# Kernel tuning notes

Measured on AMD Instinct MI355X. Metric: run time of the kernel, lower is better.

Reference implementation:

```python
import jax, jax.numpy as jnp
import numpy as np

MEMORY_SIZE = 512
EMBED_DIM = 768
BATCH, SEQ = 4, 8192


def setup_inputs() -> dict:
    key = jax.random.key(0)
    k1, k2 = jax.random.split(key)
    hidden_states = jax.random.normal(k1, (BATCH, SEQ, EMBED_DIM), dtype=jnp.float32)
    memory = jax.random.normal(k2, (MEMORY_SIZE, EMBED_DIM), dtype=jnp.float32)
    return {"hidden_states": hidden_states, "memory": memory}


def reference(hidden_states, memory):
    # importance[s] = mean over batch of L2 norm of hidden_states[b, s, :]
    importance = jnp.linalg.norm(hidden_states, axis=-1).mean(axis=0)  # [S]
    k = min(MEMORY_SIZE, importance.shape[0])  # static
    _, topk_idx = jax.lax.top_k(importance, k)  # [k]
    # gather per-token batch-mean vectors and scatter into first k memory slots
    mean_h = hidden_states.mean(axis=0)  # [S, D]
    new_memory = memory.at[:k].set(mean_h[topk_idx])  # [M, D]
    return new_memory
```

## Files before the change

kernel.cpp:

```cpp
#include <hip/hip_runtime.h>
#include <stdint.h>

#define S_TOK 8192
#define D_DIM 768
#define B_SZ  4
#define K_TOP 512
#define NSLICE 32
#define SLICE (S_TOK / NSLICE)

__global__ __launch_bounds__(256) void importance_kernel(const float4* __restrict__ h4,
                                                         uint32_t* __restrict__ imp_u) {
    const int D4 = D_DIM / 4;
    const size_t SB = (size_t)S_TOK * D4;
    const int wave = (blockIdx.x * blockDim.x + threadIdx.x) >> 6;
    const int lane = threadIdx.x & 63;
    const float4* r = h4 + (size_t)wave * D4 + lane;

    float4 v0 = r[0 * SB + 0],  v1 = r[0 * SB + 64],  v2 = r[0 * SB + 128];
    float4 v3 = r[1 * SB + 0],  v4 = r[1 * SB + 64],  v5 = r[1 * SB + 128];
    float4 v6 = r[2 * SB + 0],  v7 = r[2 * SB + 64],  v8 = r[2 * SB + 128];
    float4 v9 = r[3 * SB + 0],  vA = r[3 * SB + 64],  vB = r[3 * SB + 128];

    float d0 = v0.x * v0.x + v0.y * v0.y + v0.z * v0.z + v0.w * v0.w;
    float d1 = v1.x * v1.x + v1.y * v1.y + v1.z * v1.z + v1.w * v1.w;
    float d2 = v2.x * v2.x + v2.y * v2.y + v2.z * v2.z + v2.w * v2.w;
    float d3 = v3.x * v3.x + v3.y * v3.y + v3.z * v3.z + v3.w * v3.w;
    float d4 = v4.x * v4.x + v4.y * v4.y + v4.z * v4.z + v4.w * v4.w;
    float d5 = v5.x * v5.x + v5.y * v5.y + v5.z * v5.z + v5.w * v5.w;
    float d6 = v6.x * v6.x + v6.y * v6.y + v6.z * v6.z + v6.w * v6.w;
    float d7 = v7.x * v7.x + v7.y * v7.y + v7.z * v7.z + v7.w * v7.w;
    float d8 = v8.x * v8.x + v8.y * v8.y + v8.z * v8.z + v8.w * v8.w;
    float d9 = v9.x * v9.x + v9.y * v9.y + v9.z * v9.z + v9.w * v9.w;
    float dA = vA.x * vA.x + vA.y * vA.y + vA.z * vA.z + vA.w * vA.w;
    float dB = vB.x * vB.x + vB.y * vB.y + vB.z * vB.z + vB.w * vB.w;

    float a0 = d0 + d1 + d2;
    float a1 = d3 + d4 + d5;
    float a2 = d6 + d7 + d8;
    float a3 = d9 + dA + dB;

#pragma unroll
    for (int off = 32; off >= 1; off >>= 1) {
        a0 += __shfl_xor(a0, off);
        a1 += __shfl_xor(a1, off);
        a2 += __shfl_xor(a2, off);
        a3 += __shfl_xor(a3, off);
    }
    if (lane == 0) {
        float acc = sqrtf(a0) + sqrtf(a1) + sqrtf(a2) + sqrtf(a3);
        imp_u[wave] = __float_as_uint(acc * 0.25f);
    }
}

__global__ __launch_bounds__(256) void rank_kernel(const uint32_t* __restrict__ imp_u,
                                                   uint32_t* __restrict__ partial) {
    const int grp = blockIdx.x >> 5;
    const int c   = blockIdx.x & 31;
    const int s   = grp * 256 + threadIdx.x;
    const uint32_t ks = imp_u[s];
    const uint4* slice4 = (const uint4*)(imp_u + c * SLICE);
    uint32_t cnt = 0;
#pragma unroll 8
    for (int j4 = 0; j4 < SLICE / 4; ++j4) {
        uint4 kv = slice4[j4];
        const int jb = c * SLICE + j4 * 4;
        cnt += (kv.x > ks || (kv.x == ks && (jb + 0) < s)) ? 1u : 0u;
        cnt += (kv.y > ks || (kv.y == ks && (jb + 1) < s)) ? 1u : 0u;
        cnt += (kv.z > ks || (kv.z == ks && (jb + 2) < s)) ? 1u : 0u;
        cnt += (kv.w > ks || (kv.w == ks && (jb + 3) < s)) ? 1u : 0u;
    }
    partial[c * S_TOK + s] = cnt;
}

__global__ __launch_bounds__(256) void summap_kernel(const uint32_t* __restrict__ partial,
                                                     int* __restrict__ map) {
    const int s = blockIdx.x * 256 + threadIdx.x;
    uint32_t r = 0;
#pragma unroll
    for (int c = 0; c < NSLICE; ++c) r += partial[c * S_TOK + s];
    if (r < K_TOP) map[r] = s;
}

__global__ __launch_bounds__(192) void gather_kernel(const float4* __restrict__ h4,
                                                     const int* __restrict__ map,
                                                     float4* __restrict__ out4) {
    const int D4 = D_DIM / 4;
    const size_t SD4 = (size_t)S_TOK * D4;
    const int idx = map[blockIdx.x];
    const float4* base = h4 + (size_t)idx * D4;
    const int d = threadIdx.x;
    float4 a = base[d];
    float4 b = base[d + SD4];
    float4 c = base[d + 2 * SD4];
    float4 e = base[d + 3 * SD4];
    float4 r;
    r.x = 0.25f * (a.x + b.x + c.x + e.x);
    r.y = 0.25f * (a.y + b.y + c.y + e.y);
    r.z = 0.25f * (a.z + b.z + c.z + e.z);
    r.w = 0.25f * (a.w + b.w + c.w + e.w);
    out4[(size_t)blockIdx.x * D4 + d] = r;
}

extern "C" void kernel_launch(void* const* d_in, const int* in_sizes, int n_in,
                              void* d_out, int out_size, void* d_ws, size_t ws_size,
                              hipStream_t stream) {
    const float* h = (const float*)d_in[0];
    float* out = (float*)d_out;
    uint32_t* imp_u = (uint32_t*)d_ws;
    uint32_t* partial = (uint32_t*)((char*)d_ws + S_TOK * sizeof(uint32_t));
    int* map = (int*)((char*)d_ws + S_TOK * sizeof(uint32_t) + NSLICE * S_TOK * sizeof(uint32_t));

    importance_kernel<<<S_TOK / 4, 256, 0, stream>>>((const float4*)h, imp_u);
    rank_kernel<<<NSLICE * (S_TOK / 256), 256, 0, stream>>>(imp_u, partial);
    summap_kernel<<<S_TOK / 256, 256, 0, stream>>>(partial, map);
    gather_kernel<<<K_TOP, 192, 0, stream>>>((const float4*)h, map, (float4*)out);
}
```

Before: 40.52 us.

## Split importance pass into nontemporal-load and global-to-LDS kernels

The importance reduction is split in two. The first 5632 tokens use nontemporal vector loads. The remaining tokens go through a second kernel that streams rows into LDS with global_load_lds before reducing. The aim is to keep the L2/MALL from filling with streamed activations and to exercise a second load path. The cost is an extra kernel launch, serialized on the same stream, plus 48KB of LDS per block, which limits occupancy for that part.

New measurement: 43.52 us. 1.07x slower.

```diff
diff --git a/kernel.cpp b/kernel.cpp
--- a/kernel.cpp
+++ b/kernel.cpp
@@ -7,38 +7,39 @@
 #define K_TOP 512
 #define NSLICE 32
 #define SLICE (S_TOK / NSLICE)
+#define NT_TOK 5632
 
-__global__ __launch_bounds__(256) void importance_kernel(const float4* __restrict__ h4,
-                                                         uint32_t* __restrict__ imp_u) {
+typedef float f4v __attribute__((ext_vector_type(4)));
+
+__device__ __forceinline__ float sq4(f4v v) {
+    return v[0] * v[0] + v[1] * v[1] + v[2] * v[2] + v[3] * v[3];
+}
+
+__global__ __launch_bounds__(256) void importance_nt_kernel(const f4v* __restrict__ h4,
+                                                            uint32_t* __restrict__ imp_u) {
     const int D4 = D_DIM / 4;
     const size_t SB = (size_t)S_TOK * D4;
     const int wave = (blockIdx.x * blockDim.x + threadIdx.x) >> 6;
     const int lane = threadIdx.x & 63;
-    const float4* r = h4 + (size_t)wave * D4 + lane;
+    const f4v* r = h4 + (size_t)wave * D4 + lane;
 
-    float4 v0 = r[0 * SB + 0],  v1 = r[0 * SB + 64],  v2 = r[0 * SB + 128];
-    float4 v3 = r[1 * SB + 0],  v4 = r[1 * SB + 64],  v5 = r[1 * SB + 128];
-    float4 v6 = r[2 * SB + 0],  v7 = r[2 * SB + 64],  v8 = r[2 * SB + 128];
-    float4 v9 = r[3 * SB + 0],  vA = r[3 * SB + 64],  vB = r[3 * SB + 128];
+    f4v v0 = __builtin_nontemporal_load(r);
+    f4v v1 = __builtin_nontemporal_load(r + 64);
+    f4v v2 = __builtin_nontemporal_load(r + 128);
+    f4v v3 = __builtin_nontemporal_load(r + SB);
+    f4v v4 = __builtin_nontemporal_load(r + SB + 64);
+    f4v v5 = __builtin_nontemporal_load(r + SB + 128);
+    f4v v6 = __builtin_nontemporal_load(r + 2 * SB);
+    f4v v7 = __builtin_nontemporal_load(r + 2 * SB + 64);
+    f4v v8 = __builtin_nontemporal_load(r + 2 * SB + 128);
+    f4v v9 = __builtin_nontemporal_load(r + 3 * SB);
+    f4v vA = __builtin_nontemporal_load(r + 3 * SB + 64);
+    f4v vB = __builtin_nontemporal_load(r + 3 * SB + 128);
 
-    float d0 = v0.x * v0.x + v0.y * v0.y + v0.z * v0.z + v0.w * v0.w;
-    float d1 = v1.x * v1.x + v1.y * v1.y + v1.z * v1.z + v1.w * v1.w;
-    float d2 = v2.x * v2.x + v2.y * v2.y + v2.z * v2.z + v2.w * v2.w;
-    float d3 = v3.x * v3.x + v3.y * v3.y + v3.z * v3.z + v3.w * v3.w;
-    float d4 = v4.x * v4.x + v4.y * v4.y + v4.z * v4.z + v4.w * v4.w;
-    float d5 = v5.x * v5.x + v5.y * v5.y + v5.z * v5.z + v5.w * v5.w;
-    float d6 = v6.x * v6.x + v6.y * v6.y + v6.z * v6.z + v6.w * v6.w;
-    float d7 = v7.x * v7.x + v7.y * v7.y + v7.z * v7.z + v7.w * v7.w;
-    float d8 = v8.x * v8.x + v8.y * v8.y + v8.z * v8.z + v8.w * v8.w;
-    float d9 = v9.x * v9.x + v9.y * v9.y + v9.z * v9.z + v9.w * v9.w;
-    float dA = vA.x * vA.x + vA.y * vA.y + vA.z * vA.z + vA.w * vA.w;
-    float dB = vB.x * vB.x + vB.y * vB.y + vB.z * vB.z + vB.w * vB.w;
-
-    float a0 = d0 + d1 + d2;
-    float a1 = d3 + d4 + d5;
-    float a2 = d6 + d7 + d8;
-    float a3 = d9 + dA + dB;
-
+    float a0 = sq4(v0) + sq4(v1) + sq4(v2);
+    float a1 = sq4(v3) + sq4(v4) + sq4(v5);
+    float a2 = sq4(v6) + sq4(v7) + sq4(v8);
+    float a3 = sq4(v9) + sq4(vA) + sq4(vB);
 #pragma unroll
     for (int off = 32; off >= 1; off >>= 1) {
         a0 += __shfl_xor(a0, off);
@@ -49,6 +50,59 @@
     if (lane == 0) {
         float acc = sqrtf(a0) + sqrtf(a1) + sqrtf(a2) + sqrtf(a3);
         imp_u[wave] = __float_as_uint(acc * 0.25f);
+    }
+}
+
+#define AS1C(p) ((const __attribute__((address_space(1))) void*)(p))
+#define AS3(p)  ((__attribute__((address_space(3))) void*)(p))
+
+__global__ __launch_bounds__(256) void importance_glds_kernel(const float* __restrict__ h,
+                                                              uint32_t* __restrict__ imp_u) {
+    __shared__ char smem[4 * 12 * 1024];
+    const int w = threadIdx.x >> 6;
+    const int lane = threadIdx.x & 63;
+    const int s = NT_TOK + blockIdx.x * 4 + w;
+    char* base = smem + w * 12288;
+
+#pragma unroll
+    for (int b = 0; b < B_SZ; ++b) {
+#pragma unroll
+        for (int p = 0; p < 3; ++p) {
+            const float* g = h + ((size_t)b * S_TOK + (size_t)s) * D_DIM + p * 256 + lane * 4;
+            __builtin_amdgcn_global_load_lds(AS1C(g), AS3(base + (b * 3 + p) * 1024), 16, 0, 0);
+        }
+    }
+    asm volatile("s_waitcnt vmcnt(0)" ::: "memory");
+
+    float a0, a1, a2, a3;
+    {
+        f4v u0 = *(const f4v*)(base + 0 * 1024 + lane * 16);
+        f4v u1 = *(const f4v*)(base + 1 * 1024 + lane * 16);
+        f4v u2 = *(const f4v*)(base + 2 * 1024 + lane * 16);
+        a0 = sq4(u0) + sq4(u1) + sq4(u2);
+        f4v u3 = *(const f4v*)(base + 3 * 1024 + lane * 16);
+        f4v u4 = *(const f4v*)(base + 4 * 1024 + lane * 16);
+        f4v u5 = *(const f4v*)(base + 5 * 1024 + lane * 16);
+        a1 = sq4(u3) + sq4(u4) + sq4(u5);
+        f4v u6 = *(const f4v*)(base + 6 * 1024 + lane * 16);
+        f4v u7 = *(const f4v*)(base + 7 * 1024 + lane * 16);
+        f4v u8 = *(const f4v*)(base + 8 * 1024 + lane * 16);
+        a2 = sq4(u6) + sq4(u7) + sq4(u8);
+        f4v u9 = *(const f4v*)(base + 9 * 1024 + lane * 16);
+        f4v uA = *(const f4v*)(base + 10 * 1024 + lane * 16);
+        f4v uB = *(const f4v*)(base + 11 * 1024 + lane * 16);
+        a3 = sq4(u9) + sq4(uA) + sq4(uB);
+    }
+#pragma unroll
+    for (int off = 32; off >= 1; off >>= 1) {
+        a0 += __shfl_xor(a0, off);
+        a1 += __shfl_xor(a1, off);
+        a2 += __shfl_xor(a2, off);
+        a3 += __shfl_xor(a3, off);
+    }
+    if (lane == 0) {
+        float acc = sqrtf(a0) + sqrtf(a1) + sqrtf(a2) + sqrtf(a3);
+        imp_u[s] = __float_as_uint(acc * 0.25f);
     }
 }
 
@@ -110,7 +164,8 @@
     uint32_t* partial = (uint32_t*)((char*)d_ws + S_TOK * sizeof(uint32_t));
     int* map = (int*)((char*)d_ws + S_TOK * sizeof(uint32_t) + NSLICE * S_TOK * sizeof(uint32_t));
 
-    importance_kernel<<<S_TOK / 4, 256, 0, stream>>>((const float4*)h, imp_u);
+    importance_nt_kernel<<<NT_TOK / 4, 256, 0, stream>>>((const f4v*)h, imp_u);
+    importance_glds_kernel<<<(S_TOK - NT_TOK) / 4, 256, 0, stream>>>(h, imp_u);
     rank_kernel<<<NSLICE * (S_TOK / 256), 256, 0, stream>>>(imp_u, partial);
     summap_kernel<<<S_TOK / 256, 256, 0, stream>>>(partial, map);
     gather_kernel<<<K_TOP, 192, 0, stream>>>((const float4*)h, map, (float4*)out);
```

## Fuse rank counting, rank summation and gather into one kernel

Applied to the files above, without the earlier changes.

Replaces the three-kernel rank/summap/gather chain with a single kernel where each block ranks 16 tokens across 16 slices, reduces partial counts in shared memory, and directly gathers and writes the batch-mean rows of tokens that land in the top-k. This removes two kernel launches and the global partial/map buffers. The trade-off is that gather work is now unevenly spread, with some blocks serially processing several winning tokens while others do none, and 64 of 256 threads sit idle during the gather.

After: 41.80 us (median of 2 runs). +3.2%, slower.

```diff
diff --git a/kernel.cpp b/kernel.cpp
--- a/kernel.cpp
+++ b/kernel.cpp
@@ -5,8 +5,6 @@
 #define D_DIM 768
 #define B_SZ  4
 #define K_TOP 512
-#define NSLICE 32
-#define SLICE (S_TOK / NSLICE)
 
 __global__ __launch_bounds__(256) void importance_kernel(const float4* __restrict__ h4,
                                                          uint32_t* __restrict__ imp_u) {
@@ -38,7 +36,6 @@
     float a1 = d3 + d4 + d5;
     float a2 = d6 + d7 + d8;
     float a3 = d9 + dA + dB;
-
 #pragma unroll
     for (int off = 32; off >= 1; off >>= 1) {
         a0 += __shfl_xor(a0, off);
@@ -52,53 +49,66 @@
     }
 }
 
-__global__ __launch_bounds__(256) void rank_kernel(const uint32_t* __restrict__ imp_u,
-                                                   uint32_t* __restrict__ partial) {
-    const int grp = blockIdx.x >> 5;
-    const int c   = blockIdx.x & 31;
-    const int s   = grp * 256 + threadIdx.x;
+__global__ __launch_bounds__(256) void rank_gather_kernel(const uint32_t* __restrict__ imp_u,
+                                                          const float4* __restrict__ h4,
+                                                          float4* __restrict__ out4) {
+    const int tid = threadIdx.x;
+    const int tt = tid & 15;
+    const int sl = tid >> 4;
+    const int s = blockIdx.x * 16 + tt;
+    __shared__ uint32_t s_part[16][17];
+    __shared__ int s_wtok[16];
+    __shared__ int s_wrank[16];
+    __shared__ int s_nw;
+
     const uint32_t ks = imp_u[s];
-    const uint4* slice4 = (const uint4*)(imp_u + c * SLICE);
+    const uint4* sp = (const uint4*)(imp_u + sl * 512);
     uint32_t cnt = 0;
 #pragma unroll 8
-    for (int j4 = 0; j4 < SLICE / 4; ++j4) {
-        uint4 kv = slice4[j4];
-        const int jb = c * SLICE + j4 * 4;
+    for (int j4 = 0; j4 < 128; ++j4) {
+        uint4 kv = sp[j4];
+        const int jb = sl * 512 + j4 * 4;
         cnt += (kv.x > ks || (kv.x == ks && (jb + 0) < s)) ? 1u : 0u;
         cnt += (kv.y > ks || (kv.y == ks && (jb + 1) < s)) ? 1u : 0u;
         cnt += (kv.z > ks || (kv.z == ks && (jb + 2) < s)) ? 1u : 0u;
         cnt += (kv.w > ks || (kv.w == ks && (jb + 3) < s)) ? 1u : 0u;
     }
-    partial[c * S_TOK + s] = cnt;
-}
+    s_part[sl][tt] = cnt;
+    if (tid == 0) s_nw = 0;
+    __syncthreads();
 
-__global__ __launch_bounds__(256) void summap_kernel(const uint32_t* __restrict__ partial,
-                                                     int* __restrict__ map) {
-    const int s = blockIdx.x * 256 + threadIdx.x;
-    uint32_t r = 0;
+    if (tid < 16) {
+        uint32_t r = 0;
 #pragma unroll
-    for (int c = 0; c < NSLICE; ++c) r += partial[c * S_TOK + s];
-    if (r < K_TOP) map[r] = s;
-}
+        for (int k = 0; k < 16; ++k) r += s_part[k][tid];
+        if (r < K_TOP) {
+            int w = atomicAdd(&s_nw, 1);
+            s_wtok[w] = blockIdx.x * 16 + tid;
+            s_wrank[w] = (int)r;
+        }
+    }
+    __syncthreads();
 
-__global__ __launch_bounds__(192) void gather_kernel(const float4* __restrict__ h4,
-                                                     const int* __restrict__ map,
-                                                     float4* __restrict__ out4) {
+    const int nw = s_nw;
     const int D4 = D_DIM / 4;
-    const size_t SD4 = (size_t)S_TOK * D4;
-    const int idx = map[blockIdx.x];
-    const float4* base = h4 + (size_t)idx * D4;
-    const int d = threadIdx.x;
-    float4 a = base[d];
-    float4 b = base[d + SD4];
-    float4 c = base[d + 2 * SD4];
-    float4 e = base[d + 3 * SD4];
-    float4 r;
-    r.x = 0.25f * (a.x + b.x + c.x + e.x);
-    r.y = 0.25f * (a.y + b.y + c.y + e.y);
-    r.z = 0.25f * (a.z + b.z + c.z + e.z);
-    r.w = 0.25f * (a.w + b.w + c.w + e.w);
-    out4[(size_t)blockIdx.x * D4 + d] = r;
+    const size_t SB = (size_t)S_TOK * D4;
+    for (int w = 0; w < nw; ++w) {
+        const int idx = s_wtok[w];
+        const int rk = s_wrank[w];
+        if (tid < D4) {
+            const float4* base = h4 + (size_t)idx * D4;
+            float4 a = base[tid];
+            float4 b = base[tid + SB];
+            float4 c = base[tid + 2 * SB];
+            float4 e = base[tid + 3 * SB];
+            float4 r4;
+            r4.x = 0.25f * (a.x + b.x + c.x + e.x);
+            r4.y = 0.25f * (a.y + b.y + c.y + e.y);
+            r4.z = 0.25f * (a.z + b.z + c.z + e.z);
+            r4.w = 0.25f * (a.w + b.w + c.w + e.w);
+            out4[(size_t)rk * D4 + tid] = r4;
+        }
+    }
 }
 
 extern "C" void kernel_launch(void* const* d_in, const int* in_sizes, int n_in,
@@ -107,11 +117,7 @@
     const float* h = (const float*)d_in[0];
     float* out = (float*)d_out;
     uint32_t* imp_u = (uint32_t*)d_ws;
-    uint32_t* partial = (uint32_t*)((char*)d_ws + S_TOK * sizeof(uint32_t));
-    int* map = (int*)((char*)d_ws + S_TOK * sizeof(uint32_t) + NSLICE * S_TOK * sizeof(uint32_t));
 
     importance_kernel<<<S_TOK / 4, 256, 0, stream>>>((const float4*)h, imp_u);
-    rank_kernel<<<NSLICE * (S_TOK / 256), 256, 0, stream>>>(imp_u, partial);
-    summap_kernel<<<S_TOK / 256, 256, 0, stream>>>(partial, map);
-    gather_kernel<<<K_TOP, 192, 0, stream>>>((const float4*)h, map, (float4*)out);
+    rank_gather_kernel<<<K_TOP, 256, 0, stream>>>(imp_u, (const float4*)h, (float4*)out);
 }
```
